# Performance work log

Measured on AMD Instinct MI355X. Metric: run time of the kernel, lower is better.

Reference implementation:

```python
import jax, jax.numpy as jnp
import numpy as np

N = 50000
E = 400000
IN = 128
OUT = 128
HID = 32
HEADS = 8
NEG_SLOPE = 0.2

_DIMS_IN = [IN, HID * HEADS, HID * HEADS, HID * HEADS]
_HEADS = [HEADS, HEADS, HEADS, 1]
_CH = [HID, HID, HID, OUT]


def setup_inputs() -> dict:
    key = jax.random.key(0)
    ks = list(jax.random.split(key, 32))
    kit = iter(ks)

    def p(shape, s=0.05):
        return (jax.random.normal(next(kit), shape, dtype=jnp.float32) * s)

    inp = {}
    inp["x"] = jax.random.normal(next(kit), (N, IN), dtype=jnp.float32)
    inp["edge_index"] = jax.random.randint(next(kit), (2, E), 0, N, dtype=jnp.int32)
    for i in range(4):
        hc = _HEADS[i] * _CH[i]
        inp[f"Wl{i}"] = p((hc, _DIMS_IN[i]))
        inp[f"bl{i}"] = p((hc,))
        inp[f"Wr{i}"] = p((hc, _DIMS_IN[i]))
        inp[f"br{i}"] = p((hc,))
        inp[f"att{i}"] = p((_HEADS[i], _CH[i]))
        inp[f"b{i}"] = p((hc,))
    return inp


def _gatv2_conv(x, src, dst, Wl, bl, Wr, br, att, bias, concat):
    # PyG GATv2Conv (share_weights=False, add_self_loops handled by caller).
    n = x.shape[0]
    H, C = att.shape
    xl = (x @ Wl.T + bl).reshape(n, H, C)  # source-side transform
    xr = (x @ Wr.T + br).reshape(n, H, C)  # dest-side transform
    e = jax.nn.leaky_relu(xl[src] + xr[dst], NEG_SLOPE)  # [E, H, C]
    logits = jnp.einsum('ehc,hc->eh', e, att)            # [E, H]
    # per-destination softmax (numerically stable via segment max)
    m = jax.ops.segment_max(logits, dst, num_segments=n)
    p = jnp.exp(logits - m[dst])
    denom = jax.ops.segment_sum(p, dst, num_segments=n)
    alpha = p / denom[dst]                                # [E, H]
    out = jax.ops.segment_sum(alpha[:, :, None] * xl[src], dst, num_segments=n)  # [N, H, C]
    out = out.reshape(n, H * C) if concat else out.mean(axis=1)
    return out + bias


def reference(x, edge_index, Wl0, bl0, Wr0, br0, att0, b0,
              Wl1, bl1, Wr1, br1, att1, b1,
              Wl2, bl2, Wr2, br2, att2, b2,
              Wl3, bl3, Wr3, br3, att3, b3):
    loop = jnp.arange(N, dtype=edge_index.dtype)  # default add_self_loops=True
    src = jnp.concatenate([edge_index[0], loop])
    dst = jnp.concatenate([edge_index[1], loop])
    layers = [
        (Wl0, bl0, Wr0, br0, att0, b0, True),
        (Wl1, bl1, Wr1, br1, att1, b1, True),
        (Wl2, bl2, Wr2, br2, att2, b2, True),
        (Wl3, bl3, Wr3, br3, att3, b3, False),
    ]
    h = x
    for params in layers[:-1]:
        res = h
        h = _gatv2_conv(h, src, dst, *params)
        h = jax.nn.elu(h)  # dropout is identity in eval mode
        if res.shape == h.shape:
            h = h + res
    return _gatv2_conv(h, src, dst, *layers[-1])
```

## Files before the change

kernel.cpp:

```cpp
#include <hip/hip_runtime.h>
#include <hip/hip_bf16.h>

constexpr int NN = 50000;
constexpr int NE = 400000;
constexpr int NE2 = NE + NN;
constexpr float NEG_SLOPE = 0.2f;

typedef __attribute__((ext_vector_type(8))) __bf16 bf16x8;
typedef __attribute__((ext_vector_type(4))) float f32x4;

__device__ inline float bf2f(unsigned short u) { return __uint_as_float(((unsigned)u) << 16); }
__device__ inline unsigned short f2bf(float f) {
    unsigned x = __float_as_uint(f);
    return (unsigned short)((x + 0x7fffu + ((x >> 16) & 1u)) >> 16);
}

__device__ inline void gload16(const unsigned short* g, unsigned short* l) {
    __builtin_amdgcn_global_load_lds(
        (const __attribute__((address_space(1))) unsigned int*)(g),
        (__attribute__((address_space(3))) unsigned int*)(l), 16, 0, 0);
}

__global__ void count_deg(const int* __restrict__ ei, int* __restrict__ deg) {
    int e = blockIdx.x * blockDim.x + threadIdx.x;
    if (e >= NE2) return;
    int dst = (e < NE) ? ei[NE + e] : (e - NE);
    atomicAdd(&deg[dst], 1);
}

__global__ __launch_bounds__(1024) void scan_deg(const int* __restrict__ deg,
                                                 int* __restrict__ row_ptr,
                                                 int* __restrict__ cursor) {
    __shared__ int wsum[16];
    int t = threadIdx.x, lane = t & 63, w = t >> 6;
    int carry = 0;
    for (int base = 0; base < NN; base += 1024) {
        int i = base + t;
        int v = (i < NN) ? deg[i] : 0;
        int x = v;
        #pragma unroll
        for (int off = 1; off < 64; off <<= 1) {
            int y = __shfl_up(x, off);
            if (lane >= off) x += y;
        }
        if (lane == 63) wsum[w] = x;
        __syncthreads();
        if (w == 0 && lane < 16) {
            int s = wsum[lane];
            #pragma unroll
            for (int off = 1; off < 16; off <<= 1) {
                int y = __shfl_up(s, off);
                if (lane >= off) s += y;
            }
            wsum[lane] = s;
        }
        __syncthreads();
        int woff = (w == 0) ? 0 : wsum[w - 1];
        int incl = x + woff;
        if (i < NN) {
            int excl = carry + incl - v;
            row_ptr[i] = excl;
            cursor[i] = excl;
        }
        carry += wsum[15];
        __syncthreads();
    }
    if (t == 0) row_ptr[NN] = carry;
}

__global__ void scatter_edges(const int* __restrict__ ei, int* __restrict__ cursor,
                              int* __restrict__ csr_src) {
    int e = blockIdx.x * blockDim.x + threadIdx.x;
    if (e >= NE2) return;
    int src, dst;
    if (e < NE) { src = ei[e]; dst = ei[NE + e]; }
    else        { src = dst = e - NE; }
    int pos = atomicAdd(&cursor[dst], 1);
    csr_src[pos] = src;
}

__global__ void f32_to_bf16(const float* __restrict__ in, unsigned short* __restrict__ out, int n4) {
    int i = blockIdx.x * blockDim.x + threadIdx.x;
    if (i >= n4) return;
    float4 v = *(const float4*)(in + 4 * (size_t)i);
    ushort4 o;
    o.x = f2bf(v.x); o.y = f2bf(v.y); o.z = f2bf(v.z); o.w = f2bf(v.w);
    *(ushort4*)(out + 4 * (size_t)i) = o;
}

__global__ void conv_weights(const float* __restrict__ w0l, const float* __restrict__ w0r,
                             const float* __restrict__ w1l, const float* __restrict__ w1r,
                             const float* __restrict__ w2l, const float* __restrict__ w2r,
                             const float* __restrict__ w3l, const float* __restrict__ w3r,
                             unsigned short* __restrict__ out) {
    int i = blockIdx.x * blockDim.x + threadIdx.x;
    const float* src; int base;
    if      (i < 8192)  { src = w0l; base = 0; }
    else if (i < 16384) { src = w0r; base = 8192; }
    else if (i < 32768) { src = w1l; base = 16384; }
    else if (i < 49152) { src = w1r; base = 32768; }
    else if (i < 65536) { src = w2l; base = 49152; }
    else if (i < 81920) { src = w2r; base = 65536; }
    else if (i < 90112) { src = w3l; base = 81920; }
    else                { src = w3r; base = 90112; }
    float4 v = ((const float4*)src)[i - base];
    ushort4 o;
    o.x = f2bf(v.x); o.y = f2bf(v.y); o.z = f2bf(v.z); o.w = f2bf(v.w);
    ((ushort4*)out)[i] = o;
}

#define GBM 128
#define GBN 128
#define GBK 64

__global__ __launch_bounds__(256) void gemm_fused(const unsigned short* __restrict__ A,
                                                  const unsigned short* __restrict__ Wc,
                                                  const float* __restrict__ bl,
                                                  const float* __restrict__ br,
                                                  unsigned short* __restrict__ outl,
                                                  unsigned short* __restrict__ outr,
                                                  int M, int Nhalf, int K, int lognx) {
    __shared__ __align__(16) unsigned short Alds[GBM * GBK];
    __shared__ __align__(16) unsigned short Wlds[GBN * GBK];
    const int nwg = gridDim.x;
    const int q = nwg >> 3, r8 = nwg & 7;
    const int xcd = blockIdx.x & 7, off = blockIdx.x >> 3;
    const int wg = (xcd < r8 ? xcd * (q + 1) : r8 * (q + 1) + (xcd - r8) * q) + off;
    const int nx = 1 << lognx;
    const int bm = (wg >> lognx) * GBM, bn = (wg & (nx - 1)) * GBN;

    const int tid = threadIdx.x;
    const int lane = tid & 63, wave = tid >> 6;
    const int wr = wave >> 1, wc = wave & 1;
    const int lrow = lane & 15, kgrp = lane >> 4;

    f32x4 acc[4][4] = {};

    for (int k0 = 0; k0 < K; k0 += GBK) {
        #pragma unroll
        for (int i = 0; i < 4; ++i) {
            int p = i * 256 + tid;
            int r = p >> 3, ck = p & 7;
            int sck = ck ^ (r & 7);
            int ga = bm + r; ga = (ga < M) ? ga : (M - 1);
            unsigned short* la = &Alds[(unsigned)(i * 256 + wave * 64) * 8];
            gload16(A + (size_t)ga * K + k0 + sck * 8, la);
            unsigned short* lw = &Wlds[(unsigned)(i * 256 + wave * 64) * 8];
            gload16(Wc + (size_t)(bn + r) * K + k0 + sck * 8, lw);
        }
        __syncthreads();
        #pragma unroll
        for (int kk = 0; kk < GBK; kk += 32) {
            bf16x8 av[4], bv[4];
            #pragma unroll
            for (int i = 0; i < 4; ++i) {
                int ar = wr * 64 + i * 16 + lrow;
                int ch = ((kk >> 3) + kgrp) ^ (ar & 7);
                av[i] = *(const bf16x8*)(&Alds[ar * GBK + ch * 8]);
            }
            #pragma unroll
            for (int j = 0; j < 4; ++j) {
                int brw = wc * 64 + j * 16 + lrow;
                int ch = ((kk >> 3) + kgrp) ^ (brw & 7);
                bv[j] = *(const bf16x8*)(&Wlds[brw * GBK + ch * 8]);
            }
            #pragma unroll
            for (int i = 0; i < 4; ++i)
                #pragma unroll
                for (int j = 0; j < 4; ++j)
                    acc[i][j] = __builtin_amdgcn_mfma_f32_16x16x32_bf16(bv[j], av[i], acc[i][j], 0, 0, 0);
        }
        __syncthreads();
    }

    const int half = (bn >= Nhalf) ? 1 : 0;
    unsigned short* outp = half ? outr : outl;
    const float* bp = half ? br : bl;
    const int cb = bn - half * Nhalf + wc * 64;
    #pragma unroll
    for (int i = 0; i < 4; ++i) {
        int row = bm + wr * 64 + i * 16 + lrow;
        if (row < M) {
            #pragma unroll
            for (int j = 0; j < 4; ++j) {
                int col = cb + j * 16 + kgrp * 4;
                float4 bb = *(const float4*)(bp + col);
                ushort4 o;
                o.x = f2bf(acc[i][j][0] + bb.x);
                o.y = f2bf(acc[i][j][1] + bb.y);
                o.z = f2bf(acc[i][j][2] + bb.z);
                o.w = f2bf(acc[i][j][3] + bb.w);
                *(ushort4*)(outp + (size_t)row * Nhalf + col) = o;
            }
        }
    }
}

template <int H, int C, int VEC, int NW, bool DO_ELU, bool DO_RES, bool OUT_F32>
__global__ __launch_bounds__(128) void gat_edge(
        const unsigned short* __restrict__ xl,
        const unsigned short* __restrict__ xr,
        const float* __restrict__ att, const float* __restrict__ bias,
        const unsigned short* __restrict__ res, void* __restrict__ outp,
        const int* __restrict__ row_ptr, const int* __restrict__ csr_src) {
    constexpr int HC = H * C;
    constexpr int T = HC / VEC;
    constexpr int RW = C / VEC;
    __shared__ float smem[NW * T * (2 + VEC)];
    const int n = blockIdx.x;
    const int w = threadIdx.x / T;
    const int t = threadIdx.x % T;
    const int ch = VEC * t;
    const size_t base_r = (size_t)n * HC + ch;

    float xrv[VEC], av[VEC];
    if constexpr (VEC == 4) {
        ushort4 u = *(const ushort4*)(xr + base_r);
        xrv[0] = bf2f(u.x); xrv[1] = bf2f(u.y); xrv[2] = bf2f(u.z); xrv[3] = bf2f(u.w);
        float4 a4 = *(const float4*)(att + ch);
        av[0] = a4.x; av[1] = a4.y; av[2] = a4.z; av[3] = a4.w;
    } else {
        ushort2 u = *(const ushort2*)(xr + base_r);
        xrv[0] = bf2f(u.x); xrv[1] = bf2f(u.y);
        float2 a2 = *(const float2*)(att + ch);
        av[0] = a2.x; av[1] = a2.y;
    }

    float m = -1e30f, d = 0.f, acc[VEC];
    #pragma unroll
    for (int v = 0; v < VEC; ++v) acc[v] = 0.f;

    const int beg = row_ptr[n], end = row_ptr[n + 1];
    int e = beg + w;
    for (; e + NW < end; e += 2 * NW) {
        int s0 = csr_src[e], s1 = csr_src[e + NW];
        float x0[VEC], x1[VEC];
        if constexpr (VEC == 4) {
            ushort4 u0 = *(const ushort4*)(xl + (size_t)s0 * HC + ch);
            ushort4 u1 = *(const ushort4*)(xl + (size_t)s1 * HC + ch);
            x0[0] = bf2f(u0.x); x0[1] = bf2f(u0.y); x0[2] = bf2f(u0.z); x0[3] = bf2f(u0.w);
            x1[0] = bf2f(u1.x); x1[1] = bf2f(u1.y); x1[2] = bf2f(u1.z); x1[3] = bf2f(u1.w);
        } else {
            ushort2 u0 = *(const ushort2*)(xl + (size_t)s0 * HC + ch);
            ushort2 u1 = *(const ushort2*)(xl + (size_t)s1 * HC + ch);
            x0[0] = bf2f(u0.x); x0[1] = bf2f(u0.y);
            x1[0] = bf2f(u1.x); x1[1] = bf2f(u1.y);
        }
        float p0 = 0.f, p1 = 0.f;
        #pragma unroll
        for (int v = 0; v < VEC; ++v) {
            float u0 = x0[v] + xrv[v]; u0 = fmaxf(u0, u0 * NEG_SLOPE);
            float u1 = x1[v] + xrv[v]; u1 = fmaxf(u1, u1 * NEG_SLOPE);
            p0 = fmaf(u0, av[v], p0);
            p1 = fmaf(u1, av[v], p1);
        }
        #pragma unroll
        for (int mm = RW / 2; mm >= 1; mm >>= 1) {
            p0 += __shfl_xor(p0, mm);
            p1 += __shfl_xor(p1, mm);
        }
        float mn = fmaxf(m, fmaxf(p0, p1));
        float sc = __expf(m - mn), e0 = __expf(p0 - mn), e1 = __expf(p1 - mn);
        d = d * sc + e0 + e1;
        #pragma unroll
        for (int v = 0; v < VEC; ++v)
            acc[v] = fmaf(acc[v], sc, fmaf(e0, x0[v], e1 * x1[v]));
        m = mn;
    }
    if (e < end) {
        int s0 = csr_src[e];
        float x0[VEC];
        if constexpr (VEC == 4) {
            ushort4 u0 = *(const ushort4*)(xl + (size_t)s0 * HC + ch);
            x0[0] = bf2f(u0.x); x0[1] = bf2f(u0.y); x0[2] = bf2f(u0.z); x0[3] = bf2f(u0.w);
        } else {
            ushort2 u0 = *(const ushort2*)(xl + (size_t)s0 * HC + ch);
            x0[0] = bf2f(u0.x); x0[1] = bf2f(u0.y);
        }
        float p0 = 0.f;
        #pragma unroll
        for (int v = 0; v < VEC; ++v) {
            float u0 = x0[v] + xrv[v]; u0 = fmaxf(u0, u0 * NEG_SLOPE);
            p0 = fmaf(u0, av[v], p0);
        }
        #pragma unroll
        for (int mm = RW / 2; mm >= 1; mm >>= 1) p0 += __shfl_xor(p0, mm);
        float mn = fmaxf(m, p0);
        float sc = __expf(m - mn), e0 = __expf(p0 - mn);
        d = d * sc + e0;
        #pragma unroll
        for (int v = 0; v < VEC; ++v) acc[v] = fmaf(acc[v], sc, e0 * x0[v]);
        m = mn;
    }

    float* st = &smem[(w * T + t) * (2 + VEC)];
    st[0] = m; st[1] = d;
    #pragma unroll
    for (int v = 0; v < VEC; ++v) st[2 + v] = acc[v];
    __syncthreads();
    if (w == 0) {
        #pragma unroll
        for (int o = 1; o < NW; ++o) {
            const float* so = &smem[(o * T + t) * (2 + VEC)];
            float mo = so[0], dd = so[1];
            float mn = fmaxf(m, mo);
            float s0 = __expf(m - mn), s1 = __expf(mo - mn);
            d = d * s0 + dd * s1;
            #pragma unroll
            for (int v = 0; v < VEC; ++v) acc[v] = acc[v] * s0 + so[2 + v] * s1;
            m = mn;
        }
        float inv = 1.f / d;
        float o_[VEC];
        if constexpr (VEC == 4) {
            float4 b4 = *(const float4*)(bias + ch);
            o_[0] = acc[0] * inv + b4.x; o_[1] = acc[1] * inv + b4.y;
            o_[2] = acc[2] * inv + b4.z; o_[3] = acc[3] * inv + b4.w;
        } else {
            float2 b2 = *(const float2*)(bias + ch);
            o_[0] = acc[0] * inv + b2.x; o_[1] = acc[1] * inv + b2.y;
        }
        if constexpr (DO_ELU) {
            #pragma unroll
            for (int v = 0; v < VEC; ++v) o_[v] = o_[v] > 0.f ? o_[v] : __expf(o_[v]) - 1.f;
        }
        if constexpr (DO_RES) {
            if constexpr (VEC == 4) {
                ushort4 ru = *(const ushort4*)(res + base_r);
                o_[0] += bf2f(ru.x); o_[1] += bf2f(ru.y); o_[2] += bf2f(ru.z); o_[3] += bf2f(ru.w);
            } else {
                ushort2 ru = *(const ushort2*)(res + base_r);
                o_[0] += bf2f(ru.x); o_[1] += bf2f(ru.y);
            }
        }
        if constexpr (OUT_F32) {
            if constexpr (VEC == 4)
                *(float4*)((float*)outp + base_r) = make_float4(o_[0], o_[1], o_[2], o_[3]);
            else
                *(float2*)((float*)outp + base_r) = make_float2(o_[0], o_[1]);
        } else {
            if constexpr (VEC == 4) {
                ushort4 u;
                u.x = f2bf(o_[0]); u.y = f2bf(o_[1]); u.z = f2bf(o_[2]); u.w = f2bf(o_[3]);
                *(ushort4*)((unsigned short*)outp + base_r) = u;
            } else {
                ushort2 u;
                u.x = f2bf(o_[0]); u.y = f2bf(o_[1]);
                *(ushort2*)((unsigned short*)outp + base_r) = u;
            }
        }
    }
}

extern "C" void kernel_launch(void* const* d_in, const int* in_sizes, int n_in,
                              void* d_out, int out_size, void* d_ws, size_t ws_size,
                              hipStream_t stream) {
    const float* x  = (const float*)d_in[0];
    const int*   ei = (const int*)d_in[1];
    auto P = [&](int layer, int j) { return (const float*)d_in[2 + 6 * layer + j]; };

    unsigned short* x_bf = (unsigned short*)d_ws;
    unsigned short* h0 = x_bf + (size_t)NN * 128;
    unsigned short* h1 = h0 + (size_t)NN * 256;
    unsigned short* xl = h1 + (size_t)NN * 256;
    unsigned short* xr = xl + (size_t)NN * 256;
    unsigned short* Wb = xr + (size_t)NN * 256;
    int* csr_src = (int*)(Wb + 393216);
    int* row_ptr = csr_src + NE2;
    int* cursor  = row_ptr + (NN + 1);
    int* deg     = cursor + NN;

    hipMemsetAsync(deg, 0, NN * sizeof(int), stream);
    int eb = (NE2 + 255) / 256;
    count_deg<<<eb, 256, 0, stream>>>(ei, deg);
    scan_deg<<<1, 1024, 0, stream>>>(deg, row_ptr, cursor);
    scatter_edges<<<eb, 256, 0, stream>>>(ei, cursor, csr_src);

    conv_weights<<<384, 256, 0, stream>>>(P(0, 0), P(0, 2), P(1, 0), P(1, 2),
                                          P(2, 0), P(2, 2), P(3, 0), P(3, 2), Wb);
    int n4 = NN * 128 / 4;
    f32_to_bf16<<<(n4 + 255) / 256, 256, 0, stream>>>(x, x_bf, n4);

    const int mb = (NN + GBM - 1) / GBM;
    const int nwgL = 4 * mb, nwgLast = 2 * mb;

    gemm_fused<<<nwgL, 256, 0, stream>>>(x_bf, Wb + 0,      P(0, 1), P(0, 3), xl, xr, NN, 256, 128, 2);
    gat_edge<8, 32, 4, 2, true, false, false><<<NN, 128, 0, stream>>>(xl, xr, P(0, 4), P(0, 5),
                                                                      nullptr, h0, row_ptr, csr_src);
    gemm_fused<<<nwgL, 256, 0, stream>>>(h0,   Wb + 65536,  P(1, 1), P(1, 3), xl, xr, NN, 256, 256, 2);
    gat_edge<8, 32, 4, 2, true, true, false><<<NN, 128, 0, stream>>>(xl, xr, P(1, 4), P(1, 5),
                                                                     h0, h1, row_ptr, csr_src);
    gemm_fused<<<nwgL, 256, 0, stream>>>(h1,   Wb + 196608, P(2, 1), P(2, 3), xl, xr, NN, 256, 256, 2);
    gat_edge<8, 32, 4, 2, true, true, false><<<NN, 128, 0, stream>>>(xl, xr, P(2, 4), P(2, 5),
                                                                     h1, h0, row_ptr, csr_src);
    gemm_fused<<<nwgLast, 256, 0, stream>>>(h0, Wb + 327680, P(3, 1), P(3, 3), xl, xr, NN, 128, 256, 1);
    gat_edge<1, 128, 4, 4, false, false, true><<<NN, 128, 0, stream>>>(xl, xr, P(3, 4), P(3, 5),
                                                                       nullptr, d_out, row_ptr, csr_src);
}
```

Baseline: 424.9 us.

## Rewrite GAT edge kernel to one node per wave with lazy rescale; double-buffer GEMM

The edge aggregation kernel now assigns one destination node per wave with 8 bf16 channels per lane. The per-wave slices merge through shuffles instead of shared memory and a block barrier, and exponentials use exp2 with log2e folded into the attention weights. Online-softmax rescaling is skipped unless the new max exceeds the running max by a threshold, which cuts exp and multiply work per edge. The GEMM gets double-buffered LDS tiles so the next k-tile loads while the current one is computed, and the degree scan becomes a single pass with per-thread chunks. The lazy rescale lets unnormalised values grow by up to 2^11.5 before rescaling, which carries a small precision risk.

Result: slower. 468.4 us (+10.2%).

```diff
diff --git a/kernel.cpp b/kernel.cpp
--- a/kernel.cpp
+++ b/kernel.cpp
@@ -5,15 +5,19 @@
 constexpr int NE = 400000;
 constexpr int NE2 = NE + NN;
 constexpr float NEG_SLOPE = 0.2f;
+constexpr float LOG2E = 1.44269504f;
 
 typedef __attribute__((ext_vector_type(8))) __bf16 bf16x8;
 typedef __attribute__((ext_vector_type(4))) float f32x4;
+typedef __attribute__((ext_vector_type(2))) float f32x2;
 
 __device__ inline float bf2f(unsigned short u) { return __uint_as_float(((unsigned)u) << 16); }
 __device__ inline unsigned short f2bf(float f) {
     unsigned x = __float_as_uint(f);
     return (unsigned short)((x + 0x7fffu + ((x >> 16) & 1u)) >> 16);
 }
+__device__ inline float bflo(unsigned u) { return __uint_as_float(u << 16); }
+__device__ inline float bfhi(unsigned u) { return __uint_as_float(u & 0xffff0000u); }
 
 __device__ inline void gload16(const unsigned short* g, unsigned short* l) {
     __builtin_amdgcn_global_load_lds(
@@ -31,41 +35,44 @@
 __global__ __launch_bounds__(1024) void scan_deg(const int* __restrict__ deg,
                                                  int* __restrict__ row_ptr,
                                                  int* __restrict__ cursor) {
+    constexpr int CH = (NN + 1023) / 1024;
     __shared__ int wsum[16];
-    int t = threadIdx.x, lane = t & 63, w = t >> 6;
-    int carry = 0;
-    for (int base = 0; base < NN; base += 1024) {
-        int i = base + t;
-        int v = (i < NN) ? deg[i] : 0;
-        int x = v;
-        #pragma unroll
-        for (int off = 1; off < 64; off <<= 1) {
-            int y = __shfl_up(x, off);
-            if (lane >= off) x += y;
-        }
-        if (lane == 63) wsum[w] = x;
-        __syncthreads();
-        if (w == 0 && lane < 16) {
-            int s = wsum[lane];
-            #pragma unroll
-            for (int off = 1; off < 16; off <<= 1) {
-                int y = __shfl_up(s, off);
-                if (lane >= off) s += y;
-            }
-            wsum[lane] = s;
-        }
-        __syncthreads();
-        int woff = (w == 0) ? 0 : wsum[w - 1];
-        int incl = x + woff;
-        if (i < NN) {
-            int excl = carry + incl - v;
-            row_ptr[i] = excl;
-            cursor[i] = excl;
-        }
-        carry += wsum[15];
-        __syncthreads();
-    }
-    if (t == 0) row_ptr[NN] = carry;
+    const int t = threadIdx.x, lane = t & 63, w = t >> 6;
+    const int base = t * CH;
+    int v[CH];
+    int s = 0;
+    #pragma unroll
+    for (int i = 0; i < CH; ++i) {
+        int idx = base + i;
+        int dv = (idx < NN) ? deg[idx] : 0;
+        v[i] = s;
+        s += dv;
+    }
+    int x = s;
+    #pragma unroll
+    for (int off = 1; off < 64; off <<= 1) {
+        int y = __shfl_up(x, off);
+        if (lane >= off) x += y;
+    }
+    if (lane == 63) wsum[w] = x;
+    __syncthreads();
+    if (w == 0 && lane < 16) {
+        int ss = wsum[lane];
+        #pragma unroll
+        for (int off = 1; off < 16; off <<= 1) {
+            int y = __shfl_up(ss, off);
+            if (lane >= off) ss += y;
+        }
+        wsum[lane] = ss;
+    }
+    __syncthreads();
+    const int excl = ((w == 0) ? 0 : wsum[w - 1]) + (x - s);
+    #pragma unroll
+    for (int i = 0; i < CH; ++i) {
+        int idx = base + i;
+        if (idx < NN) { int e = excl + v[i]; row_ptr[idx] = e; cursor[idx] = e; }
+    }
+    if (t == 0) row_ptr[NN] = wsum[15];
 }
 
 __global__ void scatter_edges(const int* __restrict__ ei, int* __restrict__ cursor,
@@ -120,8 +127,8 @@
                                                   unsigned short* __restrict__ outl,
                                                   unsigned short* __restrict__ outr,
                                                   int M, int Nhalf, int K, int lognx) {
-    __shared__ __align__(16) unsigned short Alds[GBM * GBK];
-    __shared__ __align__(16) unsigned short Wlds[GBN * GBK];
+    __shared__ __align__(16) unsigned short Alds[2][GBM * GBK];
+    __shared__ __align__(16) unsigned short Wlds[2][GBN * GBK];
     const int nwg = gridDim.x;
     const int q = nwg >> 3, r8 = nwg & 7;
     const int xcd = blockIdx.x & 7, off = blockIdx.x >> 3;
@@ -136,19 +143,28 @@
 
     f32x4 acc[4][4] = {};
 
-    for (int k0 = 0; k0 < K; k0 += GBK) {
+    auto stage = [&](int cur, int k0) {
         #pragma unroll
         for (int i = 0; i < 4; ++i) {
             int p = i * 256 + tid;
             int r = p >> 3, ck = p & 7;
             int sck = ck ^ (r & 7);
             int ga = bm + r; ga = (ga < M) ? ga : (M - 1);
-            unsigned short* la = &Alds[(unsigned)(i * 256 + wave * 64) * 8];
-            gload16(A + (size_t)ga * K + k0 + sck * 8, la);
-            unsigned short* lw = &Wlds[(unsigned)(i * 256 + wave * 64) * 8];
-            gload16(Wc + (size_t)(bn + r) * K + k0 + sck * 8, lw);
-        }
-        __syncthreads();
+            gload16(A + (size_t)ga * K + k0 + sck * 8,
+                    &Alds[cur][(unsigned)(i * 256 + wave * 64) * 8]);
+            gload16(Wc + (size_t)(bn + r) * K + k0 + sck * 8,
+                    &Wlds[cur][(unsigned)(i * 256 + wave * 64) * 8]);
+        }
+    };
+
+    const int nt = K >> 6;
+    stage(0, 0);
+    __syncthreads();
+    int cur = 0;
+    for (int t = 0; t < nt; ++t) {
+        if (t + 1 < nt) stage(cur ^ 1, (t + 1) * GBK);
+        const unsigned short* Ab = Alds[cur];
+        const unsigned short* Wb = Wlds[cur];
         #pragma unroll
         for (int kk = 0; kk < GBK; kk += 32) {
             bf16x8 av[4], bv[4];
@@ -156,13 +172,13 @@
             for (int i = 0; i < 4; ++i) {
                 int ar = wr * 64 + i * 16 + lrow;
                 int ch = ((kk >> 3) + kgrp) ^ (ar & 7);
-                av[i] = *(const bf16x8*)(&Alds[ar * GBK + ch * 8]);
+                av[i] = *(const bf16x8*)(&Ab[ar * GBK + ch * 8]);
             }
             #pragma unroll
             for (int j = 0; j < 4; ++j) {
                 int brw = wc * 64 + j * 16 + lrow;
                 int ch = ((kk >> 3) + kgrp) ^ (brw & 7);
-                bv[j] = *(const bf16x8*)(&Wlds[brw * GBK + ch * 8]);
+                bv[j] = *(const bf16x8*)(&Wb[brw * GBK + ch * 8]);
             }
             #pragma unroll
             for (int i = 0; i < 4; ++i)
@@ -171,6 +187,7 @@
                     acc[i][j] = __builtin_amdgcn_mfma_f32_16x16x32_bf16(bv[j], av[i], acc[i][j], 0, 0, 0);
         }
         __syncthreads();
+        cur ^= 1;
     }
 
     const int half = (bn >= Nhalf) ? 1 : 0;
@@ -196,158 +213,180 @@
     }
 }
 
-template <int H, int C, int VEC, int NW, bool DO_ELU, bool DO_RES, bool OUT_F32>
-__global__ __launch_bounds__(128) void gat_edge(
+template <int HC, int C, bool DO_ELU, bool DO_RES, bool OUT_F32>
+__global__ __launch_bounds__(128) void gat_edge8(
         const unsigned short* __restrict__ xl,
         const unsigned short* __restrict__ xr,
         const float* __restrict__ att, const float* __restrict__ bias,
         const unsigned short* __restrict__ res, void* __restrict__ outp,
         const int* __restrict__ row_ptr, const int* __restrict__ csr_src) {
-    constexpr int HC = H * C;
-    constexpr int T = HC / VEC;
-    constexpr int RW = C / VEC;
-    __shared__ float smem[NW * T * (2 + VEC)];
-    const int n = blockIdx.x;
-    const int w = threadIdx.x / T;
-    const int t = threadIdx.x % T;
-    const int ch = VEC * t;
+    constexpr int T = HC / 8;
+    constexpr int NSL = 64 / T;
+    constexpr int RW = C / 8;
+    constexpr float THR = 11.54f;
+
+    const int lane = threadIdx.x & 63;
+    const int n = __builtin_amdgcn_readfirstlane((blockIdx.x << 1) | (threadIdx.x >> 6));
+    const int w = lane / T;
+    const int t = lane % T;
+    const int ch = t * 8;
     const size_t base_r = (size_t)n * HC + ch;
 
-    float xrv[VEC], av[VEC];
-    if constexpr (VEC == 4) {
-        ushort4 u = *(const ushort4*)(xr + base_r);
-        xrv[0] = bf2f(u.x); xrv[1] = bf2f(u.y); xrv[2] = bf2f(u.z); xrv[3] = bf2f(u.w);
-        float4 a4 = *(const float4*)(att + ch);
-        av[0] = a4.x; av[1] = a4.y; av[2] = a4.z; av[3] = a4.w;
-    } else {
-        ushort2 u = *(const ushort2*)(xr + base_r);
-        xrv[0] = bf2f(u.x); xrv[1] = bf2f(u.y);
-        float2 a2 = *(const float2*)(att + ch);
-        av[0] = a2.x; av[1] = a2.y;
-    }
-
-    float m = -1e30f, d = 0.f, acc[VEC];
-    #pragma unroll
-    for (int v = 0; v < VEC; ++v) acc[v] = 0.f;
-
+    f32x2 xr2[4], av2[4], acc2[4];
+    {
+        uint4 u = *(const uint4*)(xr + base_r);
+        xr2[0] = f32x2{bflo(u.x), bfhi(u.x)};
+        xr2[1] = f32x2{bflo(u.y), bfhi(u.y)};
+        xr2[2] = f32x2{bflo(u.z), bfhi(u.z)};
+        xr2[3] = f32x2{bflo(u.w), bfhi(u.w)};
+        float4 a0 = *(const float4*)(att + ch);
+        float4 a1 = *(const float4*)(att + ch + 4);
+        av2[0] = f32x2{a0.x, a0.y} * LOG2E;
+        av2[1] = f32x2{a0.z, a0.w} * LOG2E;
+        av2[2] = f32x2{a1.x, a1.y} * LOG2E;
+        av2[3] = f32x2{a1.z, a1.w} * LOG2E;
+        #pragma unroll
+        for (int qi = 0; qi < 4; ++qi) acc2[qi] = f32x2{0.f, 0.f};
+    }
+
+    float m = -1e30f, d = 0.f;
     const int beg = row_ptr[n], end = row_ptr[n + 1];
     int e = beg + w;
-    for (; e + NW < end; e += 2 * NW) {
-        int s0 = csr_src[e], s1 = csr_src[e + NW];
-        float x0[VEC], x1[VEC];
-        if constexpr (VEC == 4) {
-            ushort4 u0 = *(const ushort4*)(xl + (size_t)s0 * HC + ch);
-            ushort4 u1 = *(const ushort4*)(xl + (size_t)s1 * HC + ch);
-            x0[0] = bf2f(u0.x); x0[1] = bf2f(u0.y); x0[2] = bf2f(u0.z); x0[3] = bf2f(u0.w);
-            x1[0] = bf2f(u1.x); x1[1] = bf2f(u1.y); x1[2] = bf2f(u1.z); x1[3] = bf2f(u1.w);
-        } else {
-            ushort2 u0 = *(const ushort2*)(xl + (size_t)s0 * HC + ch);
-            ushort2 u1 = *(const ushort2*)(xl + (size_t)s1 * HC + ch);
-            x0[0] = bf2f(u0.x); x0[1] = bf2f(u0.y);
-            x1[0] = bf2f(u1.x); x1[1] = bf2f(u1.y);
-        }
-        float p0 = 0.f, p1 = 0.f;
-        #pragma unroll
-        for (int v = 0; v < VEC; ++v) {
-            float u0 = x0[v] + xrv[v]; u0 = fmaxf(u0, u0 * NEG_SLOPE);
-            float u1 = x1[v] + xrv[v]; u1 = fmaxf(u1, u1 * NEG_SLOPE);
-            p0 = fmaf(u0, av[v], p0);
-            p1 = fmaf(u1, av[v], p1);
-        }
+    for (; e + NSL < end; e += 2 * NSL) {
+        int s0 = csr_src[e], s1 = csr_src[e + NSL];
+        uint4 g0 = *(const uint4*)(xl + (size_t)s0 * HC + ch);
+        uint4 g1 = *(const uint4*)(xl + (size_t)s1 * HC + ch);
+        f32x2 x0[4], x1[4];
+        x0[0] = f32x2{bflo(g0.x), bfhi(g0.x)}; x0[1] = f32x2{bflo(g0.y), bfhi(g0.y)};
+        x0[2] = f32x2{bflo(g0.z), bfhi(g0.z)}; x0[3] = f32x2{bflo(g0.w), bfhi(g0.w)};
+        x1[0] = f32x2{bflo(g1.x), bfhi(g1.x)}; x1[1] = f32x2{bflo(g1.y), bfhi(g1.y)};
+        x1[2] = f32x2{bflo(g1.z), bfhi(g1.z)}; x1[3] = f32x2{bflo(g1.w), bfhi(g1.w)};
+        f32x2 p02 = {0.f, 0.f}, p12 = {0.f, 0.f};
+        #pragma unroll
+        for (int qi = 0; qi < 4; ++qi) {
+            f32x2 u0 = x0[qi] + xr2[qi];
+            f32x2 t0 = u0 * NEG_SLOPE;
+            u0.x = fmaxf(u0.x, t0.x); u0.y = fmaxf(u0.y, t0.y);
+            p02 = u0 * av2[qi] + p02;
+            f32x2 u1 = x1[qi] + xr2[qi];
+            f32x2 t1 = u1 * NEG_SLOPE;
+            u1.x = fmaxf(u1.x, t1.x); u1.y = fmaxf(u1.y, t1.y);
+            p12 = u1 * av2[qi] + p12;
+        }
+        float p0 = p02.x + p02.y, p1 = p12.x + p12.y;
         #pragma unroll
         for (int mm = RW / 2; mm >= 1; mm >>= 1) {
             p0 += __shfl_xor(p0, mm);
             p1 += __shfl_xor(p1, mm);
         }
-        float mn = fmaxf(m, fmaxf(p0, p1));
-        float sc = __expf(m - mn), e0 = __expf(p0 - mn), e1 = __expf(p1 - mn);
-        d = d * sc + e0 + e1;
-        #pragma unroll
-        for (int v = 0; v < VEC; ++v)
-            acc[v] = fmaf(acc[v], sc, fmaf(e0, x0[v], e1 * x1[v]));
-        m = mn;
+        float pmax = fmaxf(p0, p1);
+        if (__any(pmax > m + THR)) {
+            float mn = fmaxf(m, pmax);
+            float sc = exp2f(m - mn);
+            float e0 = exp2f(p0 - mn), e1 = exp2f(p1 - mn);
+            d = d * sc + e0 + e1;
+            f32x2 sc2 = {sc, sc}, e02 = {e0, e0}, e12 = {e1, e1};
+            #pragma unroll
+            for (int qi = 0; qi < 4; ++qi)
+                acc2[qi] = acc2[qi] * sc2 + (x0[qi] * e02 + x1[qi] * e12);
+            m = mn;
+        } else {
+            float e0 = exp2f(p0 - m), e1 = exp2f(p1 - m);
+            d += e0 + e1;
+            f32x2 e02 = {e0, e0}, e12 = {e1, e1};
+            #pragma unroll
+            for (int qi = 0; qi < 4; ++qi)
+                acc2[qi] = acc2[qi] + (x0[qi] * e02 + x1[qi] * e12);
+        }
     }
     if (e < end) {
         int s0 = csr_src[e];
-        float x0[VEC];
-        if constexpr (VEC == 4) {
-            ushort4 u0 = *(const ushort4*)(xl + (size_t)s0 * HC + ch);
-            x0[0] = bf2f(u0.x); x0[1] = bf2f(u0.y); x0[2] = bf2f(u0.z); x0[3] = bf2f(u0.w);
+        uint4 g0 = *(const uint4*)(xl + (size_t)s0 * HC + ch);
+        f32x2 x0[4];
+        x0[0] = f32x2{bflo(g0.x), bfhi(g0.x)}; x0[1] = f32x2{bflo(g0.y), bfhi(g0.y)};
+        x0[2] = f32x2{bflo(g0.z), bfhi(g0.z)}; x0[3] = f32x2{bflo(g0.w), bfhi(g0.w)};
+        f32x2 p02 = {0.f, 0.f};
+        #pragma unroll
+        for (int qi = 0; qi < 4; ++qi) {
+            f32x2 u0 = x0[qi] + xr2[qi];
+            f32x2 t0 = u0 * NEG_SLOPE;
+            u0.x = fmaxf(u0.x, t0.x); u0.y = fmaxf(u0.y, t0.y);
+            p02 = u0 * av2[qi] + p02;
+        }
+        float p0 = p02.x + p02.y;
+        #pragma unroll
+        for (int mm = RW / 2; mm >= 1; mm >>= 1) p0 += __shfl_xor(p0, mm);
+        if (__any(p0 > m + THR)) {
+            float mn = fmaxf(m, p0);
+            float sc = exp2f(m - mn);
+            float e0 = exp2f(p0 - mn);
+            d = d * sc + e0;
+            f32x2 sc2 = {sc, sc}, e02 = {e0, e0};
+            #pragma unroll
+            for (int qi = 0; qi < 4; ++qi) acc2[qi] = acc2[qi] * sc2 + x0[qi] * e02;
+            m = mn;
         } else {
-            ushort2 u0 = *(const ushort2*)(xl + (size_t)s0 * HC + ch);
-            x0[0] = bf2f(u0.x); x0[1] = bf2f(u0.y);
-        }
-        float p0 = 0.f;
-        #pragma unroll
-        for (int v = 0; v < VEC; ++v) {
-            float u0 = x0[v] + xrv[v]; u0 = fmaxf(u0, u0 * NEG_SLOPE);
-            p0 = fmaf(u0, av[v], p0);
-        }
-        #pragma unroll
-        for (int mm = RW / 2; mm >= 1; mm >>= 1) p0 += __shfl_xor(p0, mm);
-        float mn = fmaxf(m, p0);
-        float sc = __expf(m - mn), e0 = __expf(p0 - mn);
-        d = d * sc + e0;
-        #pragma unroll
-        for (int v = 0; v < VEC; ++v) acc[v] = fmaf(acc[v], sc, e0 * x0[v]);
+            float e0 = exp2f(p0 - m);
+            d += e0;
+            f32x2 e02 = {e0, e0};
+            #pragma unroll
+            for (int qi = 0; qi < 4; ++qi) acc2[qi] = acc2[qi] + x0[qi] * e02;
+        }
+    }
+
+    #pragma unroll
+    for (int st = T; st < 64; st <<= 1) {
+        float mo = __shfl_xor(m, st);
+        float do_ = __shfl_xor(d, st);
+        float ao[8];
+        #pragma unroll
+        for (int qi = 0; qi < 4; ++qi) {
+            ao[2 * qi]     = __shfl_xor(acc2[qi].x, st);
+            ao[2 * qi + 1] = __shfl_xor(acc2[qi].y, st);
+        }
+        float mn = fmaxf(m, mo);
+        float s0 = exp2f(m - mn), s1 = exp2f(mo - mn);
+        d = d * s0 + do_ * s1;
+        #pragma unroll
+        for (int qi = 0; qi < 4; ++qi) {
+            acc2[qi].x = acc2[qi].x * s0 + ao[2 * qi] * s1;
+            acc2[qi].y = acc2[qi].y * s0 + ao[2 * qi + 1] * s1;
+        }
         m = mn;
     }
 
-    float* st = &smem[(w * T + t) * (2 + VEC)];
-    st[0] = m; st[1] = d;
-    #pragma unroll
-    for (int v = 0; v < VEC; ++v) st[2 + v] = acc[v];
-    __syncthreads();
-    if (w == 0) {
-        #pragma unroll
-        for (int o = 1; o < NW; ++o) {
-            const float* so = &smem[(o * T + t) * (2 + VEC)];
-            float mo = so[0], dd = so[1];
-            float mn = fmaxf(m, mo);
-            float s0 = __expf(m - mn), s1 = __expf(mo - mn);
-            d = d * s0 + dd * s1;
-            #pragma unroll
-            for (int v = 0; v < VEC; ++v) acc[v] = acc[v] * s0 + so[2 + v] * s1;
-            m = mn;
-        }
+    if (lane < T) {
         float inv = 1.f / d;
-        float o_[VEC];
-        if constexpr (VEC == 4) {
-            float4 b4 = *(const float4*)(bias + ch);
-            o_[0] = acc[0] * inv + b4.x; o_[1] = acc[1] * inv + b4.y;
-            o_[2] = acc[2] * inv + b4.z; o_[3] = acc[3] * inv + b4.w;
+        float o[8];
+        float4 b0 = *(const float4*)(bias + ch);
+        float4 b1 = *(const float4*)(bias + ch + 4);
+        o[0] = acc2[0].x * inv + b0.x; o[1] = acc2[0].y * inv + b0.y;
+        o[2] = acc2[1].x * inv + b0.z; o[3] = acc2[1].y * inv + b0.w;
+        o[4] = acc2[2].x * inv + b1.x; o[5] = acc2[2].y * inv + b1.y;
+        o[6] = acc2[3].x * inv + b1.z; o[7] = acc2[3].y * inv + b1.w;
+        if constexpr (DO_ELU) {
+            #pragma unroll
+            for (int v = 0; v < 8; ++v)
+                o[v] = o[v] > 0.f ? o[v] : exp2f(o[v] * LOG2E) - 1.f;
+        }
+        if constexpr (DO_RES) {
+            uint4 ru = *(const uint4*)(res + base_r);
+            o[0] += bflo(ru.x); o[1] += bfhi(ru.x);
+            o[2] += bflo(ru.y); o[3] += bfhi(ru.y);
+            o[4] += bflo(ru.z); o[5] += bfhi(ru.z);
+            o[6] += bflo(ru.w); o[7] += bfhi(ru.w);
+        }
+        if constexpr (OUT_F32) {
+            float* op = (float*)outp + base_r;
+            *(float4*)(op)     = make_float4(o[0], o[1], o[2], o[3]);
+            *(float4*)(op + 4) = make_float4(o[4], o[5], o[6], o[7]);
         } else {
-            float2 b2 = *(const float2*)(bias + ch);
-            o_[0] = acc[0] * inv + b2.x; o_[1] = acc[1] * inv + b2.y;
-        }
-        if constexpr (DO_ELU) {
-            #pragma unroll
-            for (int v = 0; v < VEC; ++v) o_[v] = o_[v] > 0.f ? o_[v] : __expf(o_[v]) - 1.f;
-        }
-        if constexpr (DO_RES) {
-            if constexpr (VEC == 4) {
-                ushort4 ru = *(const ushort4*)(res + base_r);
-                o_[0] += bf2f(ru.x); o_[1] += bf2f(ru.y); o_[2] += bf2f(ru.z); o_[3] += bf2f(ru.w);
-            } else {
-                ushort2 ru = *(const ushort2*)(res + base_r);
-                o_[0] += bf2f(ru.x); o_[1] += bf2f(ru.y);
-            }
-        }
-        if constexpr (OUT_F32) {
-            if constexpr (VEC == 4)
-                *(float4*)((float*)outp + base_r) = make_float4(o_[0], o_[1], o_[2], o_[3]);
-            else
-                *(float2*)((float*)outp + base_r) = make_float2(o_[0], o_[1]);
-        } else {
-            if constexpr (VEC == 4) {
-                ushort4 u;
-                u.x = f2bf(o_[0]); u.y = f2bf(o_[1]); u.z = f2bf(o_[2]); u.w = f2bf(o_[3]);
-                *(ushort4*)((unsigned short*)outp + base_r) = u;
-            } else {
-                ushort2 u;
-                u.x = f2bf(o_[0]); u.y = f2bf(o_[1]);
-                *(ushort2*)((unsigned short*)outp + base_r) = u;
-            }
+            uint4 u;
+            u.x = (unsigned)f2bf(o[0]) | ((unsigned)f2bf(o[1]) << 16);
+            u.y = (unsigned)f2bf(o[2]) | ((unsigned)f2bf(o[3]) << 16);
+            u.z = (unsigned)f2bf(o[4]) | ((unsigned)f2bf(o[5]) << 16);
+            u.w = (unsigned)f2bf(o[6]) | ((unsigned)f2bf(o[7]) << 16);
+            *(uint4*)((unsigned short*)outp + base_r) = u;
         }
     }
 }
@@ -383,17 +422,18 @@
 
     const int mb = (NN + GBM - 1) / GBM;
     const int nwgL = 4 * mb, nwgLast = 2 * mb;
+    const int gat_g = NN / 2;
 
     gemm_fused<<<nwgL, 256, 0, stream>>>(x_bf, Wb + 0,      P(0, 1), P(0, 3), xl, xr, NN, 256, 128, 2);
-    gat_edge<8, 32, 4, 2, true, false, false><<<NN, 128, 0, stream>>>(xl, xr, P(0, 4), P(0, 5),
+    gat_edge8<256, 32, true, false, false><<<gat_g, 128, 0, stream>>>(xl, xr, P(0, 4), P(0, 5),
                                                                       nullptr, h0, row_ptr, csr_src);
     gemm_fused<<<nwgL, 256, 0, stream>>>(h0,   Wb + 65536,  P(1, 1), P(1, 3), xl, xr, NN, 256, 256, 2);
-    gat_edge<8, 32, 4, 2, true, true, false><<<NN, 128, 0, stream>>>(xl, xr, P(1, 4), P(1, 5),
+    gat_edge8<256, 32, true, true, false><<<gat_g, 128, 0, stream>>>(xl, xr, P(1, 4), P(1, 5),
                                                                      h0, h1, row_ptr, csr_src);
     gemm_fused<<<nwgL, 256, 0, stream>>>(h1,   Wb + 196608, P(2, 1), P(2, 3), xl, xr, NN, 256, 256, 2);
-    gat_edge<8, 32, 4, 2, true, true, false><<<NN, 128, 0, stream>>>(xl, xr, P(2, 4), P(2, 5),
+    gat_edge8<256, 32, true, true, false><<<gat_g, 128, 0, stream>>>(xl, xr, P(2, 4), P(2, 5),
                                                                      h1, h0, row_ptr, csr_src);
     gemm_fused<<<nwgLast, 256, 0, stream>>>(h0, Wb + 327680, P(3, 1), P(3, 3), xl, xr, NN, 128, 256, 1);
-    gat_edge<1, 128, 4, 4, false, false, true><<<NN, 128, 0, stream>>>(xl, xr, P(3, 4), P(3, 5),
+    gat_edge8<128, 128, false, false, true><<<gat_g, 128, 0, stream>>>(xl, xr, P(3, 4), P(3, 5),
                                                                        nullptr, d_out, row_ptr, csr_src);
 }
```
